# Kernel optimization log

Measured on AMD Instinct MI355X. Metric: run time of the kernel, lower is better.

Reference implementation:

```python
import jax, jax.numpy as jnp
import numpy as np

B, T, EDGE = 8, 10, 32
F1, F2 = 256, 128  # hard-coded filters in Q6Model
K3 = 3


def _conv(x, w, padding):
    # x: (B,H,W,Cin), w: (kh,kw,Cin,Cout)
    return jax.lax.conv_general_dilated(
        x, w, window_strides=(1, 1), padding=padding,
        dimension_numbers=('NHWC', 'HWIO', 'NHWC'))


def _convlstm(x_seq, Wx, Wh, b, return_sequences):
    # x_seq: (B,T,H,W,Cin); Keras ConvLSTM2D: input conv VALID, recurrent conv SAME,
    # gate order i, f, c, o. Dropout=0 -> no-op.
    Bsz = x_seq.shape[0]
    F = Wh.shape[2]
    Ho = x_seq.shape[2] - Wx.shape[0] + 1
    Wo = x_seq.shape[3] - Wx.shape[1] + 1
    h0 = jnp.zeros((Bsz, Ho, Wo, F), x_seq.dtype)

    def step(carry, x_t):
        h, c = carry
        z = _conv(x_t, Wx, 'VALID') + _conv(h, Wh, 'SAME') + b
        i, f, g, o = jnp.split(z, 4, axis=-1)
        i = jax.nn.sigmoid(i)
        f = jax.nn.sigmoid(f)
        o = jax.nn.sigmoid(o)
        c = f * c + i * jnp.tanh(g)
        h = o * jnp.tanh(c)
        return (h, c), h

    (h_last, _), ys = jax.lax.scan(step, (h0, h0), jnp.moveaxis(x_seq, 1, 0))
    if return_sequences:
        return jnp.moveaxis(ys, 0, 1)  # (B,T,Ho,Wo,F)
    return h_last  # (B,Ho,Wo,F)


def setup_inputs() -> dict:
    key = jax.random.key(0)
    ks = jax.random.split(key, 16)
    s = 0.05
    inp = {
        'x': jax.random.normal(ks[0], (B, T, EDGE, EDGE, 1), jnp.float32),
        't': jax.random.normal(ks[1], (B, 1, EDGE - 4, 64), jnp.float32),
        'loc': jax.random.normal(ks[2], (B, 1, EDGE - 4, 64), jnp.float32),
        # ConvLSTM2D layer 1: Cin=1 -> 4*F1 gates
        'Wx1': jax.random.normal(ks[3], (K3, K3, 1, 4 * F1), jnp.float32) * s,
        'Wh1': jax.random.normal(ks[4], (K3, K3, F1, 4 * F1), jnp.float32) * s,
        'b1': jnp.zeros((4 * F1,), jnp.float32),
        # ConvLSTM2D layer 2: Cin=F1 -> 4*F2 gates
        'Wx2': jax.random.normal(ks[5], (K3, K3, F1, 4 * F2), jnp.float32) * s,
        'Wh2': jax.random.normal(ks[6], (K3, K3, F2, 4 * F2), jnp.float32) * s,
        'b2': jnp.zeros((4 * F2,), jnp.float32),
        # Dense head inside convlstm Sequential
        'Wd1': jax.random.normal(ks[7], (F2, 256), jnp.float32) * s,
        'bd1': jnp.zeros((256,), jnp.float32),
        'Wd2': jax.random.normal(ks[8], (256, 64), jnp.float32) * s,
        'bd2': jnp.zeros((64,), jnp.float32),
        # fcs Sequential
        'Wf1': jax.random.normal(ks[9], (64, 64), jnp.float32) * s,
        'bf1': jnp.zeros((64,), jnp.float32),
        'Wf2': jax.random.normal(ks[10], (64, 1), jnp.float32) * s,
        'bf2': jnp.zeros((1,), jnp.float32),
    }
    return inp


def reference(x, t, loc, Wx1, Wh1, b1, Wx2, Wh2, b2,
              Wd1, bd1, Wd2, bd2, Wf1, bf1, Wf2, bf2):
    # convlstm stack
    h = _convlstm(x, Wx1, Wh1, b1, return_sequences=True)   # (B,T,30,30,256)
    h = _convlstm(h, Wx2, Wh2, b2, return_sequences=False)  # (B,28,28,128)
    h = jax.nn.relu(h @ Wd1 + bd1)                          # Dense on last axis
    h = jax.nn.relu(h @ Wd2 + bd2)                          # (B,28,28,64)
    out = jnp.concatenate([h, t, loc], axis=1)              # (B,30,28,64)
    out = jax.nn.relu(out @ Wf1 + bf1)
    out = out @ Wf2 + bf2                                   # (B,30,28,1)
    return out
```

## Files before the change

### kernel.cpp

```cpp
#include <hip/hip_runtime.h>
#include <math.h>

static constexpr int NB = 8, NT = 10, E = 32;
static constexpr int H1 = 30, W1 = 30, F1 = 256, G1 = 1024;
static constexpr int H2 = 28, W2 = 28, F2 = 128, G2 = 512;

typedef _Float16 half8 __attribute__((ext_vector_type(8)));
typedef float f32x4 __attribute__((ext_vector_type(4)));

__device__ __forceinline__ float sigf(float v){ return 1.0f/(1.0f + __expf(-v)); }

__global__ __launch_bounds__(512)
void l1_mfma(const float* __restrict__ x, const _Float16* __restrict__ Wh1t,
             const float* __restrict__ Wx1, const float* __restrict__ b1,
             const _Float16* __restrict__ h_prev, _Float16* __restrict__ h_out,
             float* __restrict__ c_st, int t)
{
    __shared__ _Float16 Alds[6*32*64];
    __shared__ _Float16 Blds[2][256*32];

    const int bid = blockIdx.x;
    const int nq  = bid & 3;
    const int rq  = (bid >> 2) & 7;
    const int b   = bid >> 5;
    const int y0  = rq*4;

    const int tid  = threadIdx.x;
    const int w    = tid >> 6;
    const int wm   = w >> 2;
    const int wn   = w & 3;
    const int lane = tid & 63;
    const int l15  = lane & 15;
    const int l16  = lane >> 4;
    const int c    = nq*64 + wn*16 + l15;

    f32x4 acc[4][4];
    #pragma unroll
    for (int mt=0; mt<4; ++mt)
        #pragma unroll
        for (int q=0; q<4; ++q) acc[mt][q] = (f32x4){0.f,0.f,0.f,0.f};

    int boff[4];
    #pragma unroll
    for (int q=0; q<4; ++q){
        int gl = q*64 + wn*16 + l15;
        boff[q] = ((gl<<6) + (l16<<4)) ^ ((gl&7)<<4);
    }

    const int rB  = tid >> 1, hB = tid & 1;
    const int gB  = (rB>>6)*256 + nq*64 + (rB&63);
    const int dB0 = ((rB<<6) + (hB<<5)) ^ ((rB&7)<<4);
    const int dB1 = ((rB<<6) + (hB<<5) + 16) ^ ((rB&7)<<4);
    uint4 pv0, pv1;

    for (int cih=0; cih<4; ++cih){
        #pragma unroll
        for (int it=0; it<3; ++it){
            int e = tid + (it<<9);
            int ci8 = e & 7, xx = (e>>3)&31, r = e>>8;
            int gy = y0 - 1 + r, gx = xx - 1;
            uint4 v = {0u,0u,0u,0u};
            if (gy >= 0 && gy < 30 && gx >= 0 && gx < 30)
                v = *(const uint4*)(const void*)(h_prev + ((size_t)((b*30+gy)*30+gx)<<8) + (cih<<6) + (ci8<<3));
            *(uint4*)(void*)((char*)Alds + (((((r<<5)+xx)<<7) + (ci8<<4)) ^ ((xx&7)<<4))) = v;
        }
        {
            const _Float16* src = Wh1t + ((size_t)gB<<8) + (cih<<6) + (hB<<4);
            pv0 = *(const uint4*)(const void*)src;
            pv1 = *(const uint4*)(const void*)(src + 8);
        }
        __syncthreads();
        {
            char* dst = (char*)Blds;
            *(uint4*)(void*)(dst + dB0) = pv0;
            *(uint4*)(void*)(dst + dB1) = pv1;
        }
        __syncthreads();
        int cur = 0;
        for (int nsl=0; nsl<18; ++nsl){
            const int nx = nsl + 1;
            if (nx < 18){
                int tap = nx>>1, cib = nx&1;
                const _Float16* src = Wh1t + ((size_t)(tap*1024 + gB)<<8) + (cih<<6) + (cib<<5) + (hB<<4);
                pv0 = *(const uint4*)(const void*)src;
                pv1 = *(const uint4*)(const void*)(src + 8);
            }
            {
                const int tap = nsl>>1, cib = nsl&1;
                const int dy = tap/3, dx = tap%3;
                half8 a[4], bb[4];
                #pragma unroll
                for (int mt=0; mt<4; ++mt){
                    int ax = ((mt&1)<<4) + l15 + dx; if (ax > 31) ax = 31;
                    int ar = 2*wm + (mt>>1) + dy;
                    a[mt] = *(const half8*)(const void*)((const char*)Alds +
                            (((((ar<<5)+ax)<<7) + (cib<<6) + (l16<<4)) ^ ((ax&7)<<4)));
                }
                const char* bp = (const char*)Blds + (cur<<14);
                #pragma unroll
                for (int q=0; q<4; ++q)
                    bb[q] = *(const half8*)(const void*)(bp + boff[q]);
                #pragma unroll
                for (int mt=0; mt<4; ++mt)
                    #pragma unroll
                    for (int q=0; q<4; ++q)
                        acc[mt][q] = __builtin_amdgcn_mfma_f32_16x16x32_f16(a[mt], bb[q], acc[mt][q], 0, 0, 0);
            }
            if (nx < 18){
                char* dst = (char*)Blds + ((cur^1)<<14);
                *(uint4*)(void*)(dst + dB0) = pv0;
                *(uint4*)(void*)(dst + dB1) = pv1;
            }
            __syncthreads();
            cur ^= 1;
        }
    }

    float wx[9][4], bq[4];
    #pragma unroll
    for (int tp=0; tp<9; ++tp)
        #pragma unroll
        for (int q=0; q<4; ++q) wx[tp][q] = Wx1[tp*G1 + q*F1 + c];
    #pragma unroll
    for (int q=0; q<4; ++q) bq[q] = b1[q*F1 + c];
    const float* xt = x + ((size_t)(b*NT + t))*E*E;
    #pragma unroll
    for (int mt=0; mt<4; ++mt){
        int py  = mt>>1;
        int pxb = ((mt&1)<<4) + (l16<<2);
        int yo  = y0 + 2*wm + py;
        #pragma unroll
        for (int r=0; r<4; ++r){
            int px = pxb + r;
            if (px < 30 && yo < 30){
                float z0 = acc[mt][0][r] + bq[0];
                float z1 = acc[mt][1][r] + bq[1];
                float z2 = acc[mt][2][r] + bq[2];
                float z3 = acc[mt][3][r] + bq[3];
                #pragma unroll
                for (int dy=0; dy<3; ++dy)
                    #pragma unroll
                    for (int dx=0; dx<3; ++dx){
                        float xv = xt[(yo+dy)*E + px+dx];
                        z0 += xv*wx[dy*3+dx][0]; z1 += xv*wx[dy*3+dx][1];
                        z2 += xv*wx[dy*3+dx][2]; z3 += xv*wx[dy*3+dx][3];
                    }
                float iv = sigf(z0), fv = sigf(z1), gv = tanhf(z2), ov = sigf(z3);
                int idx = ((b*30 + yo)*30 + px)*F1 + c;
                float cn = fv*c_st[idx] + iv*gv;
                c_st[idx] = cn;
                h_out[idx] = (_Float16)(ov*tanhf(cn));
            }
        }
    }
}

__global__ __launch_bounds__(512)
void l2_mfma(const _Float16* __restrict__ h1, const _Float16* __restrict__ Wx2t,
             const _Float16* __restrict__ Wh2t, const float* __restrict__ b2,
             const _Float16* __restrict__ h2prev, _Float16* __restrict__ h2out,
             float* __restrict__ c_st, int first)
{
    __shared__ _Float16 Alds[6*32*64];
    __shared__ _Float16 Blds[2][128*32];

    const int bid = blockIdx.x;
    const int qc  = bid & 3;
    const int t2  = bid >> 2;
    const int rq  = t2 % 7;
    const int b   = t2 / 7;
    const int y0  = rq*4;

    const int tid  = threadIdx.x;
    const int w    = tid >> 6;
    const int wm   = w >> 1;
    const int wn   = w & 1;
    const int lane = tid & 63;
    const int l15  = lane & 15;
    const int l16  = lane >> 4;
    const int c    = qc*32 + wn*16 + l15;

    f32x4 acc[2][4];
    #pragma unroll
    for (int mt=0; mt<2; ++mt)
        #pragma unroll
        for (int q=0; q<4; ++q) acc[mt][q] = (f32x4){0.f,0.f,0.f,0.f};

    int boff[4];
    #pragma unroll
    for (int q=0; q<4; ++q){
        int gl = q*32 + wn*16 + l15;
        boff[q] = ((gl<<6) + (l16<<4)) ^ ((gl&7)<<4);
    }

    const int rB = tid >> 2, qB = tid & 3;
    const int gB = (rB>>5)*128 + qc*32 + (rB&31);
    const int dB = ((rB<<6) + (qB<<4)) ^ ((rB&7)<<4);
    uint4 pv;

    for (int cih=0; cih<4; ++cih){
        #pragma unroll
        for (int it=0; it<3; ++it){
            int e = tid + (it<<9);
            int ci8 = e & 7, xx = (e>>3)&31, r = e>>8;
            int gy = y0 + r, gx = xx;
            uint4 v = {0u,0u,0u,0u};
            if (gy < 30 && gx < 30)
                v = *(const uint4*)(const void*)(h1 + ((size_t)((b*30+gy)*30+gx)<<8) + (cih<<6) + (ci8<<3));
            *(uint4*)(void*)((char*)Alds + (((((r<<5)+xx)<<7) + (ci8<<4)) ^ ((xx&7)<<4))) = v;
        }
        {
            const _Float16* src = Wx2t + ((size_t)gB<<8) + (cih<<6) + (qB<<3);
            pv = *(const uint4*)(const void*)src;
        }
        __syncthreads();
        *(uint4*)(void*)((char*)Blds + dB) = pv;
        __syncthreads();
        int cur = 0;
        for (int nsl=0; nsl<18; ++nsl){
            const int nx = nsl + 1;
            if (nx < 18){
                int tap = nx>>1, cib = nx&1;
                const _Float16* src = Wx2t + ((size_t)(tap*512 + gB)<<8) + (cih<<6) + (cib<<5) + (qB<<3);
                pv = *(const uint4*)(const void*)src;
            }
            {
                const int tap = nsl>>1, cib = nsl&1;
                const int dy = tap/3, dx = tap%3;
                half8 a[2], bb[4];
                #pragma unroll
                for (int mt=0; mt<2; ++mt){
                    int ax = (mt<<4) + l15 + dx; if (ax > 31) ax = 31;
                    int ar = wm + dy;
                    a[mt] = *(const half8*)(const void*)((const char*)Alds +
                            (((((ar<<5)+ax)<<7) + (cib<<6) + (l16<<4)) ^ ((ax&7)<<4)));
                }
                const char* bp = (const char*)Blds + (cur<<13);
                #pragma unroll
                for (int q=0; q<4; ++q)
                    bb[q] = *(const half8*)(const void*)(bp + boff[q]);
                #pragma unroll
                for (int mt=0; mt<2; ++mt)
                    #pragma unroll
                    for (int q=0; q<4; ++q)
                        acc[mt][q] = __builtin_amdgcn_mfma_f32_16x16x32_f16(a[mt], bb[q], acc[mt][q], 0, 0, 0);
            }
            if (nx < 18)
                *(uint4*)(void*)((char*)Blds + ((cur^1)<<13) + dB) = pv;
            __syncthreads();
            cur ^= 1;
        }
    }

    if (!first){
        for (int cih=0; cih<2; ++cih){
            #pragma unroll
            for (int it=0; it<3; ++it){
                int e = tid + (it<<9);
                int ci8 = e & 7, xx = (e>>3)&31, r = e>>8;
                int gy = y0 - 1 + r, gx = xx - 1;
                uint4 v = {0u,0u,0u,0u};
                if (gy >= 0 && gy < 28 && gx >= 0 && gx < 28)
                    v = *(const uint4*)(const void*)(h2prev + ((size_t)((b*28+gy)*28+gx)<<7) + (cih<<6) + (ci8<<3));
                *(uint4*)(void*)((char*)Alds + (((((r<<5)+xx)<<7) + (ci8<<4)) ^ ((xx&7)<<4))) = v;
            }
            {
                const _Float16* src = Wh2t + ((size_t)gB<<7) + (cih<<6) + (qB<<3);
                pv = *(const uint4*)(const void*)src;
            }
            __syncthreads();
            *(uint4*)(void*)((char*)Blds + dB) = pv;
            __syncthreads();
            int cur = 0;
            for (int nsl=0; nsl<18; ++nsl){
                const int nx = nsl + 1;
                if (nx < 18){
                    int tap = nx>>1, cib = nx&1;
                    const _Float16* src = Wh2t + ((size_t)(tap*512 + gB)<<7) + (cih<<6) + (cib<<5) + (qB<<3);
                    pv = *(const uint4*)(const void*)src;
                }
                {
                    const int tap = nsl>>1, cib = nsl&1;
                    const int dy = tap/3, dx = tap%3;
                    half8 a[2], bb[4];
                    #pragma unroll
                    for (int mt=0; mt<2; ++mt){
                        int ax = (mt<<4) + l15 + dx; if (ax > 31) ax = 31;
                        int ar = wm + dy;
                        a[mt] = *(const half8*)(const void*)((const char*)Alds +
                                (((((ar<<5)+ax)<<7) + (cib<<6) + (l16<<4)) ^ ((ax&7)<<4)));
                    }
                    const char* bp = (const char*)Blds + (cur<<13);
                    #pragma unroll
                    for (int q=0; q<4; ++q)
                        bb[q] = *(const half8*)(const void*)(bp + boff[q]);
                    #pragma unroll
                    for (int mt=0; mt<2; ++mt)
                        #pragma unroll
                        for (int q=0; q<4; ++q)
                            acc[mt][q] = __builtin_amdgcn_mfma_f32_16x16x32_f16(a[mt], bb[q], acc[mt][q], 0, 0, 0);
                }
                if (nx < 18)
                    *(uint4*)(void*)((char*)Blds + ((cur^1)<<13) + dB) = pv;
                __syncthreads();
                cur ^= 1;
            }
        }
    }

    float bq[4];
    #pragma unroll
    for (int q=0; q<4; ++q) bq[q] = b2[q*F2 + c];
    const int yo = y0 + wm;
    #pragma unroll
    for (int mt=0; mt<2; ++mt){
        #pragma unroll
        for (int r=0; r<4; ++r){
            int px = (mt<<4) + (l16<<2) + r;
            if (px < 28){
                float z0 = acc[mt][0][r] + bq[0];
                float z1 = acc[mt][1][r] + bq[1];
                float z2 = acc[mt][2][r] + bq[2];
                float z3 = acc[mt][3][r] + bq[3];
                float iv = sigf(z0), fv = sigf(z1), gv = tanhf(z2), ov = sigf(z3);
                int idx = ((b*28 + yo)*28 + px)*F2 + c;
                float cold = first ? 0.0f : c_st[idx];
                float cn = fv*cold + iv*gv;
                c_st[idx] = cn;
                h2out[idx] = (_Float16)(ov*tanhf(cn));
            }
        }
    }
}

__global__ __launch_bounds__(256)
void prep_t0(const float* __restrict__ Wh1, const float* __restrict__ Wx2,
             const float* __restrict__ Wh2, _Float16* __restrict__ Wh1t,
             _Float16* __restrict__ Wx2t, _Float16* __restrict__ Wh2t,
             const float* __restrict__ x, const float* __restrict__ Wx1,
             const float* __restrict__ b1, _Float16* __restrict__ h_out,
             float* __restrict__ c_st)
{
    if (blockIdx.x < 16128){
        int i = blockIdx.x*256 + threadIdx.x;
        if (i < 2359296){
            int ci = i & 255, g = (i>>8) & 1023, tap = i>>18;
            Wh1t[i] = (_Float16)Wh1[(tap*256 + ci)*1024 + g];
        } else if (i < 2359296 + 1179648){
            int j = i - 2359296;
            int ci = j & 255, g = (j>>8) & 511, tap = j>>17;
            Wx2t[j] = (_Float16)Wx2[(tap*256 + ci)*512 + g];
        } else if (i < 2359296 + 1179648 + 589824){
            int j = i - (2359296 + 1179648);
            int ci = j & 127, g = (j>>7) & 511, tap = j>>16;
            Wh2t[j] = (_Float16)Wh2[(tap*128 + ci)*512 + g];
        }
        return;
    }
    const int bid = blockIdx.x - 16128;
    const int y = bid % 30, b = bid / 30;
    const int c = threadIdx.x;
    float wx[9][4], bq[4];
    #pragma unroll
    for (int tp=0; tp<9; ++tp)
        #pragma unroll
        for (int q=0; q<4; ++q) wx[tp][q] = Wx1[tp*G1 + q*F1 + c];
    #pragma unroll
    for (int q=0; q<4; ++q) bq[q] = b1[q*F1 + c];
    const float* xt = x + ((size_t)b*NT)*E*E;
    for (int px=0; px<30; ++px){
        float z0=bq[0], z1=bq[1], z2=bq[2], z3=bq[3];
        #pragma unroll
        for (int dy=0; dy<3; ++dy)
            #pragma unroll
            for (int dx=0; dx<3; ++dx){
                float xv = xt[(y+dy)*E + px+dx];
                z0 += xv*wx[dy*3+dx][0]; z1 += xv*wx[dy*3+dx][1];
                z2 += xv*wx[dy*3+dx][2]; z3 += xv*wx[dy*3+dx][3];
            }
        float iv = sigf(z0), gv = tanhf(z2), ov = sigf(z3);
        int idx = ((b*30 + y)*30 + px)*F1 + c;
        float cn = iv*gv;
        c_st[idx] = cn;
        h_out[idx] = (_Float16)(ov*tanhf(cn));
    }
}

__global__ __launch_bounds__(256)
void dense1_k(const _Float16* __restrict__ h2, const float* __restrict__ W,
              const float* __restrict__ bv, float* __restrict__ out)
{
    __shared__ float row[F2];
    int r = blockIdx.x;
    int j = threadIdx.x;
    if (j < F2) row[j] = (float)h2[(size_t)r*F2 + j];
    __syncthreads();
    float s = bv[j];
    #pragma unroll 8
    for (int k=0; k<F2; ++k) s += row[k]*W[(size_t)k*256 + j];
    out[(size_t)r*256 + j] = s > 0.f ? s : 0.f;
}

__global__ __launch_bounds__(256)
void dense2_k(const float* __restrict__ in, const float* __restrict__ W,
              const float* __restrict__ bv, float* __restrict__ cat)
{
    int tid = threadIdx.x;
    int j  = tid & 63;
    int rl = tid >> 6;
    int r = blockIdx.x*4 + rl;
    const float* irow = in + (size_t)r*256;
    float s = bv[j];
    #pragma unroll 8
    for (int k=0; k<256; ++k) s += irow[k]*W[(size_t)k*64 + j];
    int b   = r / (H2*W2);
    int rem = r % (H2*W2);
    int yy  = rem / W2;
    int xx  = rem % W2;
    float v = s > 0.f ? s : 0.f;
    cat[(((size_t)b*30 + yy)*W2 + xx)*64 + j] = v;
}

__global__ void copy_tl_k(const float* __restrict__ tin, const float* __restrict__ lin,
                          float* __restrict__ cat)
{
    int i = blockIdx.x*blockDim.x + threadIdx.x;
    const int n = NB*W2*64;
    if (i < 2*n){
        const float* src = (i < n) ? tin : lin;
        int ii   = (i < n) ? i : i - n;
        int yrow = (i < n) ? 28 : 29;
        int b    = ii / (W2*64);
        int rem  = ii % (W2*64);
        cat[(((size_t)b*30 + yrow)*W2)*64 + rem] = src[ii];
    }
}

__global__ __launch_bounds__(256)
void fc1_k(const float* __restrict__ in, const float* __restrict__ W,
           const float* __restrict__ bv, float* __restrict__ out)
{
    int tid = threadIdx.x;
    int j  = tid & 63;
    int rl = tid >> 6;
    int r = blockIdx.x*4 + rl;
    const float* irow = in + (size_t)r*64;
    float s = bv[j];
    #pragma unroll 8
    for (int k=0; k<64; ++k) s += irow[k]*W[(size_t)k*64 + j];
    out[(size_t)r*64 + j] = s > 0.f ? s : 0.f;
}

__global__ __launch_bounds__(256)
void fc2_k(const float* __restrict__ in, const float* __restrict__ W,
           const float* __restrict__ bv, float* __restrict__ out)
{
    int tid  = threadIdx.x;
    int lane = tid & 63;
    int r = blockIdx.x*4 + (tid >> 6);
    float v = in[(size_t)r*64 + lane] * W[lane];
    #pragma unroll
    for (int s=32; s>0; s>>=1) v += __shfl_down(v, s, 64);
    if (lane == 0) out[r] = v + bv[0];
}

extern "C" void kernel_launch(void* const* d_in, const int* in_sizes, int n_in,
                              void* d_out, int out_size, void* d_ws, size_t ws_size,
                              hipStream_t stream)
{
    (void)in_sizes; (void)n_in; (void)out_size; (void)ws_size;
    const float* x   = (const float*)d_in[0];
    const float* tin = (const float*)d_in[1];
    const float* lin = (const float*)d_in[2];
    const float* Wx1 = (const float*)d_in[3];
    const float* Wh1 = (const float*)d_in[4];
    const float* b1  = (const float*)d_in[5];
    const float* Wx2 = (const float*)d_in[6];
    const float* Wh2 = (const float*)d_in[7];
    const float* b2  = (const float*)d_in[8];
    const float* Wd1 = (const float*)d_in[9];
    const float* bd1 = (const float*)d_in[10];
    const float* Wd2 = (const float*)d_in[11];
    const float* bd2 = (const float*)d_in[12];
    const float* Wf1 = (const float*)d_in[13];
    const float* bf1 = (const float*)d_in[14];
    const float* Wf2 = (const float*)d_in[15];
    const float* bf2 = (const float*)d_in[16];
    float* out = (float*)d_out;

    char* p = (char*)d_ws;
    _Float16* h1a  = (_Float16*)p; p += 3686400;
    _Float16* h1b  = (_Float16*)p; p += 3686400;
    float*    c1   = (float*)p;    p += 7372800;
    _Float16* h2a  = (_Float16*)p; p += 1605632;
    _Float16* h2b  = (_Float16*)p; p += 1605632;
    float*    c2   = (float*)p;    p += 3211264;
    _Float16* Wh1t = (_Float16*)p; p += 4718592;
    _Float16* Wx2t = (_Float16*)p; p += 2359296;
    _Float16* Wh2t = (_Float16*)p; p += 1179648;
    float* d1o = c1;
    float* cat = (float*)h1a;
    float* f1o = (float*)h1b;

    _Float16* h1w[2] = {h1a, h1b};
    _Float16* h2w[2] = {h2a, h2b};

    prep_t0<<<16368, 256, 0, stream>>>(Wh1, Wx2, Wh2, Wh1t, Wx2t, Wh2t,
                                       x, Wx1, b1, h1w[0], c1);
    l2_mfma<<<224, 512, 0, stream>>>(h1w[0], Wx2t, Wh2t, b2, h2w[0], h2w[0], c2, 1);
    for (int t=1; t<NT; ++t){
        l1_mfma<<<256, 512, 0, stream>>>(x, Wh1t, Wx1, b1, h1w[(t-1)&1], h1w[t&1], c1, t);
        l2_mfma<<<224, 512, 0, stream>>>(h1w[t&1], Wx2t, Wh2t, b2, h2w[(t-1)&1], h2w[t&1], c2, 0);
    }
    dense1_k<<<6272, 256, 0, stream>>>(h2w[1], Wd1, bd1, d1o);
    dense2_k<<<1568, 256, 0, stream>>>(d1o, Wd2, bd2, cat);
    copy_tl_k<<<(2*NB*W2*64 + 255)/256, 256, 0, stream>>>(tin, lin, cat);
    fc1_k<<<1680, 256, 0, stream>>>(cat, Wf1, bf1, f1o);
    fc2_k<<<1680, 256, 0, stream>>>(f1o, Wf2, bf2, out);
}
```

Before: 1.310 ms.

## Fuse layer-1 step t+1 with layer-2 step t in one wavefront-pipelined launch

Layer-1 and layer-2 ConvLSTM kernels become device-side bodies selected by block index inside one fused_step kernel. Each launch computes layer-1 at time t+1 alongside layer-2 at time t, since both read only h1 at time t. This halves the launch count and lets the two layers' blocks share the GPU at once, so the small 224-block layer-2 grid no longer runs alone. The costs are a larger static shared-memory footprint (57 KB, the maximum of the two), which may reduce occupancy, and some idle blocks in the grid mapping.

```diff
diff --git a/kernel.cpp b/kernel.cpp
--- a/kernel.cpp
+++ b/kernel.cpp
@@ -10,22 +10,20 @@
 
 __device__ __forceinline__ float sigf(float v){ return 1.0f/(1.0f + __expf(-v)); }
 
-__global__ __launch_bounds__(512)
-void l1_mfma(const float* __restrict__ x, const _Float16* __restrict__ Wh1t,
+__device__ __forceinline__
+void l1_body(char* smem, int nq, int sub, int tid,
+             const float* __restrict__ x, const _Float16* __restrict__ Wh1t,
              const float* __restrict__ Wx1, const float* __restrict__ b1,
              const _Float16* __restrict__ h_prev, _Float16* __restrict__ h_out,
              float* __restrict__ c_st, int t)
 {
-    __shared__ _Float16 Alds[6*32*64];
-    __shared__ _Float16 Blds[2][256*32];
-
-    const int bid = blockIdx.x;
-    const int nq  = bid & 3;
-    const int rq  = (bid >> 2) & 7;
-    const int b   = bid >> 5;
+    _Float16* Alds = (_Float16*)smem;
+    _Float16* Blds = (_Float16*)(smem + 24576);
+
+    const int rq  = sub & 7;
+    const int b   = sub >> 3;
     const int y0  = rq*4;
 
-    const int tid  = threadIdx.x;
     const int w    = tid >> 6;
     const int wm   = w >> 2;
     const int wn   = w & 3;
@@ -155,23 +153,20 @@
     }
 }
 
-__global__ __launch_bounds__(512)
-void l2_mfma(const _Float16* __restrict__ h1, const _Float16* __restrict__ Wx2t,
+__device__ __forceinline__
+void l2_body(char* smem, int qc, int sub, int tid,
+             const _Float16* __restrict__ h1, const _Float16* __restrict__ Wx2t,
              const _Float16* __restrict__ Wh2t, const float* __restrict__ b2,
              const _Float16* __restrict__ h2prev, _Float16* __restrict__ h2out,
              float* __restrict__ c_st, int first)
 {
-    __shared__ _Float16 Alds[6*32*64];
-    __shared__ _Float16 Blds[2][128*32];
-
-    const int bid = blockIdx.x;
-    const int qc  = bid & 3;
-    const int t2  = bid >> 2;
-    const int rq  = t2 % 7;
-    const int b   = t2 / 7;
+    _Float16* Alds = (_Float16*)smem;
+    _Float16* Blds = (_Float16*)(smem + 24576);
+
+    const int rq  = sub % 7;
+    const int b   = sub / 7;
     const int y0  = rq*4;
 
-    const int tid  = threadIdx.x;
     const int w    = tid >> 6;
     const int wm   = w >> 1;
     const int wn   = w & 1;
@@ -333,6 +328,38 @@
     }
 }
 
+__global__ __launch_bounds__(512)
+void fused_step(const float* __restrict__ x, const _Float16* __restrict__ Wh1t,
+                const float* __restrict__ Wx1, const float* __restrict__ b1,
+                const _Float16* __restrict__ h1_cur, _Float16* __restrict__ h1_nxt,
+                float* __restrict__ c1,
+                const _Float16* __restrict__ Wx2t, const _Float16* __restrict__ Wh2t,
+                const float* __restrict__ b2,
+                const _Float16* __restrict__ h2_prev, _Float16* __restrict__ h2_out,
+                float* __restrict__ c2, int t_next, int first)
+{
+    __shared__ char smem[57344];
+    const int bid = blockIdx.x;
+    const int xg  = bid & 7;
+    const int sub = bid >> 3;
+    if (xg >= 4){
+        l1_body(smem, xg - 4, sub, threadIdx.x, x, Wh1t, Wx1, b1, h1_cur, h1_nxt, c1, t_next);
+    } else if (sub < 56){
+        l2_body(smem, xg, sub, threadIdx.x, h1_cur, Wx2t, Wh2t, b2, h2_prev, h2_out, c2, first);
+    }
+}
+
+__global__ __launch_bounds__(512)
+void l2_mfma(const _Float16* __restrict__ h1, const _Float16* __restrict__ Wx2t,
+             const _Float16* __restrict__ Wh2t, const float* __restrict__ b2,
+             const _Float16* __restrict__ h2prev, _Float16* __restrict__ h2out,
+             float* __restrict__ c_st, int first)
+{
+    __shared__ char smem[40960];
+    const int bid = blockIdx.x;
+    l2_body(smem, bid & 3, bid >> 2, threadIdx.x, h1, Wx2t, Wh2t, b2, h2prev, h2out, c_st, first);
+}
+
 __global__ __launch_bounds__(256)
 void prep_t0(const float* __restrict__ Wh1, const float* __restrict__ Wx2,
              const float* __restrict__ Wh2, _Float16* __restrict__ Wh1t,
@@ -507,11 +534,16 @@
 
     prep_t0<<<16368, 256, 0, stream>>>(Wh1, Wx2, Wh2, Wh1t, Wx2t, Wh2t,
                                        x, Wx1, b1, h1w[0], c1);
-    l2_mfma<<<224, 512, 0, stream>>>(h1w[0], Wx2t, Wh2t, b2, h2w[0], h2w[0], c2, 1);
-    for (int t=1; t<NT; ++t){
-        l1_mfma<<<256, 512, 0, stream>>>(x, Wh1t, Wx1, b1, h1w[(t-1)&1], h1w[t&1], c1, t);
-        l2_mfma<<<224, 512, 0, stream>>>(h1w[t&1], Wx2t, Wh2t, b2, h2w[(t-1)&1], h2w[t&1], c2, 0);
-    }
+    for (int t=0; t<9; ++t){
+        fused_step<<<512, 512, 0, stream>>>(
+            x, Wh1t, Wx1, b1,
+            h1w[t&1], h1w[(t+1)&1], c1,
+            Wx2t, Wh2t, b2,
+            h2w[(t+1)&1], h2w[t&1], c2,
+            t+1, t==0);
+    }
+    l2_mfma<<<224, 512, 0, stream>>>(h1w[1], Wx2t, Wh2t, b2, h2w[0], h2w[1], c2, 0);
+
     dense1_k<<<6272, 256, 0, stream>>>(h2w[1], Wd1, bd1, d1o);
     dense2_k<<<1568, 256, 0, stream>>>(d1o, Wd2, bd2, cat);
     copy_tl_k<<<(2*NB*W2*64 + 255)/256, 256, 0, stream>>>(tin, lin, cat);
```

Measured after the change: 1.312 ms. About the same (+0.1%).
